# Kernel tuning notes

Hardware: AMD Instinct MI355X
Metric: run time of the kernel (lower is better)

## Reference

```python
import jax, jax.numpy as jnp
import numpy as np

VOCAB, EMB, HID = 120000, 64, 128
B, T = 256, 512


def _rnn_layer(inp, W_ih, b_ih, W_hh, b_hh):
    # inp: [B,T,D]. PyTorch RNN: h_t = tanh(W_ih x_t + b_ih + W_hh h_{t-1} + b_hh)
    pre = jnp.einsum('btd,hd->bth', inp, W_ih) + b_ih + b_hh  # input part hoisted out of scan
    h0 = jnp.zeros((inp.shape[0], W_hh.shape[0]), inp.dtype)

    def step(h, p_t):
        h = jnp.tanh(p_t + h @ W_hh.T)
        return h, h

    hT, outs = jax.lax.scan(step, h0, pre.transpose(1, 0, 2))  # scan over time
    return outs.transpose(1, 0, 2), hT  # [B,T,H], [B,H]


def _layernorm(x, g, b, eps=1e-5):
    mu = jnp.mean(x, axis=-1, keepdims=True)
    var = jnp.var(x, axis=-1, keepdims=True)
    return (x - mu) * jax.lax.rsqrt(var + eps) * g + b


def setup_inputs() -> dict:
    key = jax.random.key(0)
    ks = jax.random.split(key, 10)
    emb = jax.random.normal(ks[0], (VOCAB, EMB), jnp.float32) * 0.02
    emb = emb.at[0].set(0.0)  # padding_idx=0
    s_in, s_h = 1.0 / np.sqrt(HID), 1.0 / np.sqrt(HID)
    return {
        'x': jax.random.randint(ks[1], (B, T), 0, VOCAB),
        'emb': emb,
        'W_ih1': jax.random.normal(ks[2], (HID, EMB), jnp.float32) * s_in,
        'b_ih1': jnp.zeros((HID,), jnp.float32),
        'W_hh1': jax.random.normal(ks[3], (HID, HID), jnp.float32) * s_h,
        'b_hh1': jnp.zeros((HID,), jnp.float32),
        'W_ih2': jax.random.normal(ks[4], (HID, HID), jnp.float32) * s_in,
        'b_ih2': jnp.zeros((HID,), jnp.float32),
        'W_hh2': jax.random.normal(ks[5], (HID, HID), jnp.float32) * s_h,
        'b_hh2': jnp.zeros((HID,), jnp.float32),
        'ln_g': jnp.ones((HID,), jnp.float32),
        'ln_b': jnp.zeros((HID,), jnp.float32),
        'proj_W': jax.random.normal(ks[6], (HID, HID), jnp.float32) * s_h,
        'proj_b': jnp.zeros((HID,), jnp.float32),
        'on_g': jnp.ones((HID,), jnp.float32),
        'on_b': jnp.zeros((HID,), jnp.float32),
    }


def reference(x, emb, W_ih1, b_ih1, W_hh1, b_hh1, W_ih2, b_ih2, W_hh2, b_hh2,
              ln_g, ln_b, proj_W, proj_b, on_g, on_b):
    e = emb[x]                                   # [B,T,64]
    out1, _ = _rnn_layer(e, W_ih1, b_ih1, W_hh1, b_hh1)   # dropout is identity in eval
    _, h2 = _rnn_layer(out1, W_ih2, b_ih2, W_hh2, b_hh2)  # h2: [B,128] (last hidden state)
    rep = _layernorm(h2, ln_g, ln_b)
    rep = jnp.tanh(rep @ proj_W.T + proj_b)
    rep = _layernorm(rep, on_g, on_b)
    return rep
```

## Files before the change

### kernel.cpp

```cpp
#include <hip/hip_runtime.h>

#define BT (256*512)
#define HID 128
#define EMB 64
#define CH 32

__device__ __forceinline__ float fast_tanh(float x) {
    float e = __expf(2.f * x);
    return 1.f - __fdividef(2.f, e + 1.f);
}

#define OPQ(v) asm volatile("" : "+v"(v.x), "+v"(v.y), "+v"(v.z), "+v"(v.w))

#define DPPADD(v, ctrl) ((v) + __int_as_float(__builtin_amdgcn_mov_dpp(__float_as_int(v), (ctrl), 0xF, 0xF, false)))

#define RACC(P, Q, wa, wb, wc, wd) \
    P = fmaf(hv0.x, wa.x, P); Q = fmaf(hv0.y, wa.y, Q); \
    P = fmaf(hv0.z, wa.z, P); Q = fmaf(hv0.w, wa.w, Q); \
    P = fmaf(hv1.x, wb.x, P); Q = fmaf(hv1.y, wb.y, Q); \
    P = fmaf(hv1.z, wb.z, P); Q = fmaf(hv1.w, wb.w, Q); \
    P = fmaf(hv2.x, wc.x, P); Q = fmaf(hv2.y, wc.y, Q); \
    P = fmaf(hv2.z, wc.z, P); Q = fmaf(hv2.w, wc.w, Q); \
    P = fmaf(hv3.x, wd.x, P); Q = fmaf(hv3.y, wd.y, Q); \
    P = fmaf(hv3.z, wd.z, P); Q = fmaf(hv3.w, wd.w, Q);

__global__ __launch_bounds__(256)
__attribute__((amdgpu_waves_per_eu(1, 2)))
void k_embed_pre1(
    const int* __restrict__ x, const float* __restrict__ emb,
    const float* __restrict__ Wih1, const float* __restrict__ bih1,
    const float* __restrict__ bhh1, float* __restrict__ pre1)
{
    __shared__ float sA[32][128];
    __shared__ float sW[32][132];
    __shared__ int stok[128];
    const int tid = threadIdx.x;
    const int base = blockIdx.x * 128;
    const int tx = tid & 15, ty = tid >> 4;
    const int ox = tx * 8, py = ty * 8;
    const int pl = tid & 127, half = tid >> 7;
    if (tid < 128) stok[tid] = x[base + tid];
    float acc[8][8];
#pragma unroll
    for (int p = 0; p < 8; ++p)
#pragma unroll
        for (int o = 0; o < 8; ++o) acc[p][o] = 0.f;
    __syncthreads();
    const float4* ws = (const float4*)(Wih1 + (size_t)pl * EMB + half * 16);
    const float4* as = (const float4*)(emb + (size_t)stok[pl] * EMB + half * 16);
    float4 qw[2][4], qe[2][4];
#pragma unroll
    for (int kc = 0; kc < 2; ++kc)
#pragma unroll
        for (int k = 0; k < 4; ++k) {
            qw[kc][k] = ws[kc * 8 + k];
            qe[kc][k] = as[kc * 8 + k];
        }
    for (int kc = 0; kc < 2; ++kc) {
        {
            const int jb = half * 16;
#pragma unroll
            for (int k = 0; k < 4; ++k) {
                float4 q = qw[kc][k], e = qe[kc][k];
                sW[jb + 4*k + 0][pl] = q.x; sW[jb + 4*k + 1][pl] = q.y;
                sW[jb + 4*k + 2][pl] = q.z; sW[jb + 4*k + 3][pl] = q.w;
                sA[jb + 4*k + 0][pl] = e.x; sA[jb + 4*k + 1][pl] = e.y;
                sA[jb + 4*k + 2][pl] = e.z; sA[jb + 4*k + 3][pl] = e.w;
            }
        }
        __syncthreads();
#pragma unroll 4
        for (int j = 0; j < 32; ++j) {
            float4 a0 = *(const float4*)&sA[j][py];
            float4 a1 = *(const float4*)&sA[j][py + 4];
            float4 b0 = *(const float4*)&sW[j][ox];
            float4 b1 = *(const float4*)&sW[j][ox + 4];
            float av[8] = {a0.x,a0.y,a0.z,a0.w,a1.x,a1.y,a1.z,a1.w};
            float bv[8] = {b0.x,b0.y,b0.z,b0.w,b1.x,b1.y,b1.z,b1.w};
#pragma unroll
            for (int p = 0; p < 8; ++p)
#pragma unroll
                for (int o = 0; o < 8; ++o)
                    acc[p][o] = fmaf(av[p], bv[o], acc[p][o]);
        }
        __syncthreads();
    }
    float bo[8];
#pragma unroll
    for (int o = 0; o < 8; ++o) bo[o] = bih1[ox + o] + bhh1[ox + o];
#pragma unroll
    for (int p = 0; p < 8; ++p) {
        float* cp = pre1 + (size_t)(base + py + p) * HID + ox;
        *(float4*)cp       = make_float4(acc[p][0]+bo[0], acc[p][1]+bo[1], acc[p][2]+bo[2], acc[p][3]+bo[3]);
        *(float4*)(cp + 4) = make_float4(acc[p][4]+bo[4], acc[p][5]+bo[5], acc[p][6]+bo[6], acc[p][7]+bo[7]);
    }
}

__device__ inline float bsum768(float v, volatile float* sc, int tid) {
#pragma unroll
    for (int off = 32; off > 0; off >>= 1) v += __shfl_down(v, off, 64);
    __syncthreads();
    if ((tid & 63) == 0) sc[tid >> 6] = v;
    __syncthreads();
    float s = 0.f;
#pragma unroll
    for (int k = 0; k < 12; ++k) s += sc[k];
    return s;
}

__global__ __launch_bounds__(768)
__attribute__((amdgpu_waves_per_eu(1, 3)))
void k_rnn_fused(
    const float* __restrict__ pre1, const float* __restrict__ Whh1,
    const float* __restrict__ Wih2, const float* __restrict__ bih2,
    const float* __restrict__ bhh2, const float* __restrict__ Whh2,
    const float* __restrict__ ln_g, const float* __restrict__ ln_b,
    const float* __restrict__ projW, const float* __restrict__ proj_b,
    const float* __restrict__ on_g, const float* __restrict__ on_b,
    float* __restrict__ out)
{
    __shared__ __align__(16) float h1[2][160];
    __shared__ __align__(16) float h2[2][160];
    __shared__ __align__(16) float spre[CH * HID];
    __shared__ float sfin[HID];
    __shared__ float sc[12];

    const int bb   = blockIdx.x;
    const int tid  = threadIdx.x;
    const int w    = tid >> 6;
    const int lane = tid & 63;
    const bool L1  = (w < 4);
    const int  e   = lane & 7;
    const int  m   = L1 ? 0 : ((lane >> 3) & 1);
    const int  rg  = L1 ? (lane >> 3) : (lane >> 4);
    const int  rowbase = L1 ? (32 * w + rg) : (16 * (w - 4) + rg);
    const int  rstep   = L1 ? 8 : 4;
    const float* wmat  = L1 ? Whh1 : (m ? Whh2 : Wih2);

    const float4* wr0 = (const float4*)(wmat + (size_t)(rowbase            ) * HID + e * 16);
    const float4* wr1 = (const float4*)(wmat + (size_t)(rowbase +     rstep) * HID + e * 16);
    const float4* wr2 = (const float4*)(wmat + (size_t)(rowbase + 2 * rstep) * HID + e * 16);
    const float4* wr3 = (const float4*)(wmat + (size_t)(rowbase + 3 * rstep) * HID + e * 16);
    float4 w0 = wr0[0], w1 = wr0[1], w2  = wr0[2], w3  = wr0[3],
           w4 = wr1[0], w5 = wr1[1], w6  = wr1[2], w7  = wr1[3],
           w8 = wr2[0], w9 = wr2[1], w10 = wr2[2], w11 = wr2[3],
           w12= wr3[0], w13= wr3[1], w14 = wr3[2], w15 = wr3[3];
    OPQ(w0);OPQ(w1);OPQ(w2);OPQ(w3);OPQ(w4);OPQ(w5);OPQ(w6);OPQ(w7);
    OPQ(w8);OPQ(w9);OPQ(w10);OPQ(w11);OPQ(w12);OPQ(w13);OPQ(w14);OPQ(w15);

    const bool wr_en = L1 ? (e < 4) : (m == 0 && e < 4);
    const int  wrow  = rowbase + (e & 3) * rstep;
    const int  wword = ((wrow >> 4) * 20) + (wrow & 15);
    const float b2w  = (!L1 && wr_en) ? (bih2[wrow] + bhh2[wrow]) : 0.f;

    if (tid < 160) { h1[0][tid] = 0.f; h2[0][tid] = 0.f; }

    const float* srcb = (L1 || m == 0) ? &h1[0][0] : &h2[0][0];
    const float4* rp0 = (const float4*)(srcb + e * 20);
    const float4* rp1 = (const float4*)(srcb + 160 + e * 20);
    float* dstb = L1 ? &h1[0][0] : &h2[0][0];
    float* wp_e = dstb + 160 + wword;
    float* wp_o = dstb + wword;

    const float4* gsrc = (const float4*)(pre1 + (size_t)bb * 512 * HID);
    float4* spv = (float4*)spre;
    float4 pf0, pf1;
    if (tid < 512) { pf0 = gsrc[tid]; pf1 = gsrc[tid + 512]; }
    __syncthreads();

    auto do_step = [&](int t, int s, const float4* rp, float* wpt) {
        float4 hv0 = rp[0], hv1 = rp[1], hv2 = rp[2], hv3 = rp[3];
        float p0=0,q0=0,p1=0,q1=0,p2=0,q2=0,p3=0,q3=0;
        RACC(p0,q0, w0,w1,w2,w3)
        RACC(p1,q1, w4,w5,w6,w7)
        RACC(p2,q2, w8,w9,w10,w11)
        RACC(p3,q3, w12,w13,w14,w15)
        float s0 = p0+q0, s1 = p1+q1, s2 = p2+q2, s3 = p3+q3;
        s0 = DPPADD(s0, 0xB1); s1 = DPPADD(s1, 0xB1); s2 = DPPADD(s2, 0xB1); s3 = DPPADD(s3, 0xB1);
        s0 = DPPADD(s0, 0x4E); s1 = DPPADD(s1, 0x4E); s2 = DPPADD(s2, 0x4E); s3 = DPPADD(s3, 0x4E);
        s0 = DPPADD(s0, 0x141); s1 = DPPADD(s1, 0x141); s2 = DPPADD(s2, 0x141); s3 = DPPADD(s3, 0x141);
        if (!L1) {
            s0 = DPPADD(s0, 0x140); s1 = DPPADD(s1, 0x140);
            s2 = DPPADD(s2, 0x140); s3 = DPPADD(s3, 0x140);
        }
        if (wr_en) {
            float ta = (e & 1) ? s1 : s0;
            float tb = (e & 1) ? s3 : s2;
            float v  = (e & 2) ? tb : ta;
            if (L1) *wpt = fast_tanh(spre[s * HID + wrow] + v);
            else    *wpt = (t > 0) ? fast_tanh(b2w + v) : 0.f;
        }
        __syncthreads();
    };

#pragma unroll 1
    for (int c = 0; c < 512 / CH; ++c) {
        if (tid < 512) { spv[tid] = pf0; spv[tid + 512] = pf1; }
        __syncthreads();
        if (c < 512 / CH - 1 && tid < 512) {
            pf0 = gsrc[(c + 1) * 1024 + tid];
            pf1 = gsrc[(c + 1) * 1024 + tid + 512];
        }
        const int t0 = c * CH;
#pragma unroll 1
        for (int s = 0; s < CH; s += 2) {
            do_step(t0 + s,     s,     rp0, wp_e);
            do_step(t0 + s + 1, s + 1, rp1, wp_o);
        }
    }

    {
        float* wpD = L1 ? wp_e : &sfin[wrow];
        do_step(512, 0, rp0, wpD);
    }

    const int i = tid & 127;
    float hn = (tid < 128) ? sfin[i] : 0.f;
    float s1v = bsum768(hn, sc, tid);
    float s2v = bsum768(hn * hn, sc, tid);
    float mu = s1v * (1.f / 128.f);
    float var = s2v * (1.f / 128.f) - mu * mu;
    __syncthreads();
    if (tid < 128) spre[i] = (hn - mu) * rsqrtf(var + 1e-5f) * ln_g[i] + ln_b[i];
    __syncthreads();
    float pv = 0.f;
    if (tid < 128) {
        float a0 = proj_b[i], a1 = 0, a2 = 0, a3 = 0;
        const float4* hp = (const float4*)spre;
        const float4* pr = (const float4*)(projW + (size_t)i * HID);
#pragma unroll
        for (int k = 0; k < HID / 4; ++k) {
            float4 u = pr[k];
            float4 hv = hp[k];
            a0 = fmaf(hv.x, u.x, a0); a1 = fmaf(hv.y, u.y, a1);
            a2 = fmaf(hv.z, u.z, a2); a3 = fmaf(hv.w, u.w, a3);
        }
        pv = tanhf((a0 + a1) + (a2 + a3));
    }
    float t1 = bsum768(pv, sc, tid);
    float t2 = bsum768(pv * pv, sc, tid);
    float mu2 = t1 * (1.f / 128.f);
    float var2 = t2 * (1.f / 128.f) - mu2 * mu2;
    if (tid < 128)
        out[(size_t)bb * HID + i] = (pv - mu2) * rsqrtf(var2 + 1e-5f) * on_g[i] + on_b[i];
}

extern "C" void kernel_launch(void* const* d_in, const int* in_sizes, int n_in,
                              void* d_out, int out_size, void* d_ws, size_t ws_size,
                              hipStream_t stream)
{
    const int*   x     = (const int*)  d_in[0];
    const float* emb   = (const float*)d_in[1];
    const float* Wih1  = (const float*)d_in[2];
    const float* bih1  = (const float*)d_in[3];
    const float* Whh1  = (const float*)d_in[4];
    const float* bhh1  = (const float*)d_in[5];
    const float* Wih2  = (const float*)d_in[6];
    const float* bih2  = (const float*)d_in[7];
    const float* Whh2  = (const float*)d_in[8];
    const float* bhh2  = (const float*)d_in[9];
    const float* ln_g  = (const float*)d_in[10];
    const float* ln_b  = (const float*)d_in[11];
    const float* projW = (const float*)d_in[12];
    const float* projb = (const float*)d_in[13];
    const float* on_g  = (const float*)d_in[14];
    const float* on_b  = (const float*)d_in[15];

    float* pre1 = (float*)d_ws;

    k_embed_pre1<<<BT / 128, 256, 0, stream>>>(x, emb, Wih1, bih1, bhh1, pre1);
    k_rnn_fused<<<256, 768, 0, stream>>>(pre1, Whh1, Wih2, bih2, bhh2, Whh2,
                                         ln_g, ln_b, projW, projb, on_g, on_b,
                                         (float*)d_out);
}
```

Baseline: 447.9 us.

## Batch RNN scan across sequences with split-fp16 MFMA and pipelined layers

The recurrent scan now processes 16 sequences per block (16 blocks) using 16x16x32 fp16 MFMA. fp32 precision is emulated with hi/lo fp16 splits (three MFMAs per tile). The two layers and the layer-2 input projection run in separate wave roles, skewed in time and double-buffered in LDS. The pre1 layout is changed to time-major for coalesced per-step loads, and the layernorm/projection head moves to a separate kernel. This trades the per-sequence scalar FMA and DPP reductions for matrix-core throughput, but only 16 blocks run on a large GPU and there is a barrier every step.

```diff
diff --git a/kernel.cpp b/kernel.cpp
--- a/kernel.cpp
+++ b/kernel.cpp
@@ -3,26 +3,26 @@
 #define BT (256*512)
 #define HID 128
 #define EMB 64
-#define CH 32
+#define NB  16
+#define SEQ 16
+
+typedef _Float16 f16x4 __attribute__((ext_vector_type(4)));
+typedef _Float16 f16x8 __attribute__((ext_vector_type(8)));
+typedef float    f32x4 __attribute__((ext_vector_type(4)));
+
+#define MFMA(a, b, c) __builtin_amdgcn_mfma_f32_16x16x32_f16(a, b, c, 0, 0, 0)
+#define SHUF8(x, y) __builtin_shufflevector(x, y, 0, 1, 2, 3, 4, 5, 6, 7)
+#define TRRD(dst, a, OFF) asm volatile("ds_read_b64_tr_b16 %0, %1 offset:" OFF : "=v"(dst) : "v"(a))
+#define LDSR128(dst, a)   asm volatile("ds_read_b128 %0, %1" : "=v"(dst) : "v"(a))
 
 __device__ __forceinline__ float fast_tanh(float x) {
     float e = __expf(2.f * x);
     return 1.f - __fdividef(2.f, e + 1.f);
 }
 
-#define OPQ(v) asm volatile("" : "+v"(v.x), "+v"(v.y), "+v"(v.z), "+v"(v.w))
-
-#define DPPADD(v, ctrl) ((v) + __int_as_float(__builtin_amdgcn_mov_dpp(__float_as_int(v), (ctrl), 0xF, 0xF, false)))
-
-#define RACC(P, Q, wa, wb, wc, wd) \
-    P = fmaf(hv0.x, wa.x, P); Q = fmaf(hv0.y, wa.y, Q); \
-    P = fmaf(hv0.z, wa.z, P); Q = fmaf(hv0.w, wa.w, Q); \
-    P = fmaf(hv1.x, wb.x, P); Q = fmaf(hv1.y, wb.y, Q); \
-    P = fmaf(hv1.z, wb.z, P); Q = fmaf(hv1.w, wb.w, Q); \
-    P = fmaf(hv2.x, wc.x, P); Q = fmaf(hv2.y, wc.y, Q); \
-    P = fmaf(hv2.z, wc.z, P); Q = fmaf(hv2.w, wc.w, Q); \
-    P = fmaf(hv3.x, wd.x, P); Q = fmaf(hv3.y, wd.y, Q); \
-    P = fmaf(hv3.z, wd.z, P); Q = fmaf(hv3.w, wd.w, Q);
+__device__ __forceinline__ unsigned ldsoff(const void* p) {
+    return (unsigned)(unsigned long long)p;
+}
 
 __global__ __launch_bounds__(256)
 __attribute__((amdgpu_waves_per_eu(1, 2)))
@@ -90,159 +90,264 @@
     for (int o = 0; o < 8; ++o) bo[o] = bih1[ox + o] + bhh1[ox + o];
 #pragma unroll
     for (int p = 0; p < 8; ++p) {
-        float* cp = pre1 + (size_t)(base + py + p) * HID + ox;
+        const int pos = base + py + p;
+        const int bI = pos >> 9, tI = pos & 511;
+        float* cp = pre1 + ((size_t)tI * 256 + bI) * HID + ox;
         *(float4*)cp       = make_float4(acc[p][0]+bo[0], acc[p][1]+bo[1], acc[p][2]+bo[2], acc[p][3]+bo[3]);
         *(float4*)(cp + 4) = make_float4(acc[p][4]+bo[4], acc[p][5]+bo[5], acc[p][6]+bo[6], acc[p][7]+bo[7]);
     }
 }
 
-__device__ inline float bsum768(float v, volatile float* sc, int tid) {
-#pragma unroll
-    for (int off = 32; off > 0; off >>= 1) v += __shfl_down(v, off, 64);
-    __syncthreads();
-    if ((tid & 63) == 0) sc[tid >> 6] = v;
-    __syncthreads();
-    float s = 0.f;
-#pragma unroll
-    for (int k = 0; k < 12; ++k) s += sc[k];
-    return s;
-}
-
-__global__ __launch_bounds__(768)
-__attribute__((amdgpu_waves_per_eu(1, 3)))
-void k_rnn_fused(
-    const float* __restrict__ pre1, const float* __restrict__ Whh1,
+__global__ __launch_bounds__(384)
+__attribute__((amdgpu_waves_per_eu(2)))
+void k_rnn_scan(
+    const float* __restrict__ pre1T, const float* __restrict__ Whh1,
     const float* __restrict__ Wih2, const float* __restrict__ bih2,
     const float* __restrict__ bhh2, const float* __restrict__ Whh2,
-    const float* __restrict__ ln_g, const float* __restrict__ ln_b,
-    const float* __restrict__ projW, const float* __restrict__ proj_b,
-    const float* __restrict__ on_g, const float* __restrict__ on_b,
-    float* __restrict__ out)
+    float* __restrict__ h2fin)
 {
-    __shared__ __align__(16) float h1[2][160];
-    __shared__ __align__(16) float h2[2][160];
-    __shared__ __align__(16) float spre[CH * HID];
-    __shared__ float sfin[HID];
-    __shared__ float sc[12];
-
-    const int bb   = blockIdx.x;
+    __shared__ __align__(16) _Float16 hT[2][4][HID * SEQ];
+    __shared__ __align__(16) float    Pp[2][HID * SEQ];
+
     const int tid  = threadIdx.x;
-    const int w    = tid >> 6;
-    const int lane = tid & 63;
-    const bool L1  = (w < 4);
-    const int  e   = lane & 7;
-    const int  m   = L1 ? 0 : ((lane >> 3) & 1);
-    const int  rg  = L1 ? (lane >> 3) : (lane >> 4);
-    const int  rowbase = L1 ? (32 * w + rg) : (16 * (w - 4) + rg);
-    const int  rstep   = L1 ? 8 : 4;
-    const float* wmat  = L1 ? Whh1 : (m ? Whh2 : Wih2);
-
-    const float4* wr0 = (const float4*)(wmat + (size_t)(rowbase            ) * HID + e * 16);
-    const float4* wr1 = (const float4*)(wmat + (size_t)(rowbase +     rstep) * HID + e * 16);
-    const float4* wr2 = (const float4*)(wmat + (size_t)(rowbase + 2 * rstep) * HID + e * 16);
-    const float4* wr3 = (const float4*)(wmat + (size_t)(rowbase + 3 * rstep) * HID + e * 16);
-    float4 w0 = wr0[0], w1 = wr0[1], w2  = wr0[2], w3  = wr0[3],
-           w4 = wr1[0], w5 = wr1[1], w6  = wr1[2], w7  = wr1[3],
-           w8 = wr2[0], w9 = wr2[1], w10 = wr2[2], w11 = wr2[3],
-           w12= wr3[0], w13= wr3[1], w14 = wr3[2], w15 = wr3[3];
-    OPQ(w0);OPQ(w1);OPQ(w2);OPQ(w3);OPQ(w4);OPQ(w5);OPQ(w6);OPQ(w7);
-    OPQ(w8);OPQ(w9);OPQ(w10);OPQ(w11);OPQ(w12);OPQ(w13);OPQ(w14);OPQ(w15);
-
-    const bool wr_en = L1 ? (e < 4) : (m == 0 && e < 4);
-    const int  wrow  = rowbase + (e & 3) * rstep;
-    const int  wword = ((wrow >> 4) * 20) + (wrow & 15);
-    const float b2w  = (!L1 && wr_en) ? (bih2[wrow] + bhh2[wrow]) : 0.f;
-
-    if (tid < 160) { h1[0][tid] = 0.f; h2[0][tid] = 0.f; }
-
-    const float* srcb = (L1 || m == 0) ? &h1[0][0] : &h2[0][0];
-    const float4* rp0 = (const float4*)(srcb + e * 20);
-    const float4* rp1 = (const float4*)(srcb + 160 + e * 20);
-    float* dstb = L1 ? &h1[0][0] : &h2[0][0];
-    float* wp_e = dstb + 160 + wword;
-    float* wp_o = dstb + wword;
-
-    const float4* gsrc = (const float4*)(pre1 + (size_t)bb * 512 * HID);
-    float4* spv = (float4*)spre;
-    float4 pf0, pf1;
-    if (tid < 512) { pf0 = gsrc[tid]; pf1 = gsrc[tid + 512]; }
-    __syncthreads();
-
-    auto do_step = [&](int t, int s, const float4* rp, float* wpt) {
-        float4 hv0 = rp[0], hv1 = rp[1], hv2 = rp[2], hv3 = rp[3];
-        float p0=0,q0=0,p1=0,q1=0,p2=0,q2=0,p3=0,q3=0;
-        RACC(p0,q0, w0,w1,w2,w3)
-        RACC(p1,q1, w4,w5,w6,w7)
-        RACC(p2,q2, w8,w9,w10,w11)
-        RACC(p3,q3, w12,w13,w14,w15)
-        float s0 = p0+q0, s1 = p1+q1, s2 = p2+q2, s3 = p3+q3;
-        s0 = DPPADD(s0, 0xB1); s1 = DPPADD(s1, 0xB1); s2 = DPPADD(s2, 0xB1); s3 = DPPADD(s3, 0xB1);
-        s0 = DPPADD(s0, 0x4E); s1 = DPPADD(s1, 0x4E); s2 = DPPADD(s2, 0x4E); s3 = DPPADD(s3, 0x4E);
-        s0 = DPPADD(s0, 0x141); s1 = DPPADD(s1, 0x141); s2 = DPPADD(s2, 0x141); s3 = DPPADD(s3, 0x141);
-        if (!L1) {
-            s0 = DPPADD(s0, 0x140); s1 = DPPADD(s1, 0x140);
-            s2 = DPPADD(s2, 0x140); s3 = DPPADD(s3, 0x140);
-        }
-        if (wr_en) {
-            float ta = (e & 1) ? s1 : s0;
-            float tb = (e & 1) ? s3 : s2;
-            float v  = (e & 2) ? tb : ta;
-            if (L1) *wpt = fast_tanh(spre[s * HID + wrow] + v);
-            else    *wpt = (t > 0) ? fast_tanh(b2w + v) : 0.f;
+    const int w    = tid >> 6, lane = tid & 63;
+    const int role = w >> 1, half = w & 1;
+    const int col  = lane & 15;
+    const int kg   = lane >> 4;
+    const int sb   = kg * 4;
+    const int b0   = blockIdx.x * SEQ;
+
+    {
+        _Float16* z = &hT[0][0][0];
+        for (int i = tid; i < 4 * HID * SEQ; i += 384) z[i] = (_Float16)0.f;
+        for (int i = tid; i < HID * SEQ; i += 384) Pp[0][i] = 0.f;
+    }
+
+    const float* WM = (role == 0) ? Whh1 : ((role == 1) ? Wih2 : Whh2);
+    f16x8 bh[4][4], bl[4][4];
+    int outj[4];
+#pragma unroll
+    for (int j = 0; j < 4; ++j) {
+        const int out = (half * 4 + j) * 16 + col;
+        outj[j] = out;
+        const float* rp = WM + (size_t)out * HID + kg * 4;
+#pragma unroll
+        for (int kt = 0; kt < 4; ++kt) {
+            float4 a = *(const float4*)(rp + kt * 32);
+            float4 b4 = *(const float4*)(rp + kt * 32 + 16);
+            float v[8] = {a.x, a.y, a.z, a.w, b4.x, b4.y, b4.z, b4.w};
+            f16x8 hi, lo;
+#pragma unroll
+            for (int q = 0; q < 8; ++q) {
+                _Float16 h = (_Float16)v[q];
+                hi[q] = h;
+                lo[q] = (_Float16)(v[q] - (float)h);
+            }
+            bh[j][kt] = hi; bl[j][kt] = lo;
+        }
+    }
+    float b2j[4] = {0.f, 0.f, 0.f, 0.f};
+    if (role == 2) {
+#pragma unroll
+        for (int j = 0; j < 4; ++j) b2j[j] = bih2[outj[j]] + bhh2[outj[j]];
+    }
+
+    const unsigned hTb = ldsoff(&hT[0][0][0]);
+    const unsigned Ppb = ldsoff(&Pp[0][0]);
+    const int arr = (role == 2) ? 2 : 0;
+    const unsigned aHi0 = hTb + arr * 4096 + lane * 8;
+    const unsigned aHi1 = aHi0 + 16384;
+    int pjo[4];
+#pragma unroll
+    for (int j = 0; j < 4; ++j) pjo[j] = (outj[j] * 16 + sb) * 4;
+
+    float pc[4][4];
+    if (role == 0) {
+#pragma unroll
+        for (int j = 0; j < 4; ++j)
+#pragma unroll
+            for (int r = 0; r < 4; ++r)
+                pc[j][r] = pre1T[(size_t)(b0 + sb + r) * HID + outj[j]];
+    }
+    __syncthreads();
+
+    auto stepf = [&](int t, int rp) {
+        const int wp = rp ^ 1;
+        if (role == 0) {
+            if (t < 512) {
+                const unsigned ah = rp ? aHi1 : aHi0;
+                const unsigned al = ah + 4096;
+                f16x4 u0,u1,u2,u3,u4,u5,u6,u7, m0,m1,m2,m3,m4,m5,m6,m7;
+                TRRD(u0, ah, "0");    TRRD(u1, ah, "512");
+                TRRD(u2, ah, "1024"); TRRD(u3, ah, "1536");
+                TRRD(u4, ah, "2048"); TRRD(u5, ah, "2560");
+                TRRD(u6, ah, "3072"); TRRD(u7, ah, "3584");
+                TRRD(m0, al, "0");    TRRD(m1, al, "512");
+                TRRD(m2, al, "1024"); TRRD(m3, al, "1536");
+                TRRD(m4, al, "2048"); TRRD(m5, al, "2560");
+                TRRD(m6, al, "3072"); TRRD(m7, al, "3584");
+                asm volatile("s_waitcnt lgkmcnt(0)" ::: "memory");
+                __builtin_amdgcn_sched_barrier(0);
+                f16x8 Ah[4] = {SHUF8(u0,u1), SHUF8(u2,u3), SHUF8(u4,u5), SHUF8(u6,u7)};
+                f16x8 Al[4] = {SHUF8(m0,m1), SHUF8(m2,m3), SHUF8(m4,m5), SHUF8(m6,m7)};
+#pragma unroll
+                for (int j = 0; j < 4; ++j) {
+                    f32x4 c = {pc[j][0], pc[j][1], pc[j][2], pc[j][3]};
+#pragma unroll
+                    for (int kt = 0; kt < 4; ++kt) c = MFMA(Ah[kt], bh[j][kt], c);
+#pragma unroll
+                    for (int kt = 0; kt < 4; ++kt) c = MFMA(Al[kt], bh[j][kt], c);
+#pragma unroll
+                    for (int kt = 0; kt < 4; ++kt) c = MFMA(Ah[kt], bl[j][kt], c);
+                    f16x4 hi4, lo4;
+#pragma unroll
+                    for (int r = 0; r < 4; ++r) {
+                        float v = fast_tanh(c[r]);
+                        _Float16 h = (_Float16)v;
+                        hi4[r] = h;
+                        lo4[r] = (_Float16)(v - (float)h);
+                    }
+                    *(f16x4*)&hT[wp][0][outj[j] * 16 + sb] = hi4;
+                    *(f16x4*)&hT[wp][1][outj[j] * 16 + sb] = lo4;
+                }
+                const int tn = (t + 1 < 512) ? t + 1 : 511;
+                const size_t tb = (size_t)tn * 256 + b0 + sb;
+#pragma unroll
+                for (int j = 0; j < 4; ++j)
+#pragma unroll
+                    for (int r = 0; r < 4; ++r)
+                        pc[j][r] = pre1T[(tb + r) * HID + outj[j]];
+            }
+        } else if (role == 1) {
+            if (t < 513) {
+                const unsigned ah = rp ? aHi1 : aHi0;
+                const unsigned al = ah + 4096;
+                f16x4 u0,u1,u2,u3,u4,u5,u6,u7, m0,m1,m2,m3,m4,m5,m6,m7;
+                TRRD(u0, ah, "0");    TRRD(u1, ah, "512");
+                TRRD(u2, ah, "1024"); TRRD(u3, ah, "1536");
+                TRRD(u4, ah, "2048"); TRRD(u5, ah, "2560");
+                TRRD(u6, ah, "3072"); TRRD(u7, ah, "3584");
+                TRRD(m0, al, "0");    TRRD(m1, al, "512");
+                TRRD(m2, al, "1024"); TRRD(m3, al, "1536");
+                TRRD(m4, al, "2048"); TRRD(m5, al, "2560");
+                TRRD(m6, al, "3072"); TRRD(m7, al, "3584");
+                asm volatile("s_waitcnt lgkmcnt(0)" ::: "memory");
+                __builtin_amdgcn_sched_barrier(0);
+                f16x8 Ah[4] = {SHUF8(u0,u1), SHUF8(u2,u3), SHUF8(u4,u5), SHUF8(u6,u7)};
+                f16x8 Al[4] = {SHUF8(m0,m1), SHUF8(m2,m3), SHUF8(m4,m5), SHUF8(m6,m7)};
+#pragma unroll
+                for (int j = 0; j < 4; ++j) {
+                    f32x4 c = {0.f, 0.f, 0.f, 0.f};
+#pragma unroll
+                    for (int kt = 0; kt < 4; ++kt) c = MFMA(Ah[kt], bh[j][kt], c);
+#pragma unroll
+                    for (int kt = 0; kt < 4; ++kt) c = MFMA(Al[kt], bh[j][kt], c);
+#pragma unroll
+                    for (int kt = 0; kt < 4; ++kt) c = MFMA(Ah[kt], bl[j][kt], c);
+                    *(f32x4*)&Pp[wp][outj[j] * 16 + sb] = c;
+                }
+            }
+        } else {
+            const unsigned ah = rp ? aHi1 : aHi0;
+            const unsigned al = ah + 4096;
+            const unsigned pb = Ppb + rp * 8192;
+            f32x4 P0, P1, P2, P3;
+            LDSR128(P0, pb + pjo[0]); LDSR128(P1, pb + pjo[1]);
+            LDSR128(P2, pb + pjo[2]); LDSR128(P3, pb + pjo[3]);
+            f16x4 u0,u1,u2,u3,u4,u5,u6,u7, m0,m1,m2,m3,m4,m5,m6,m7;
+            TRRD(u0, ah, "0");    TRRD(u1, ah, "512");
+            TRRD(u2, ah, "1024"); TRRD(u3, ah, "1536");
+            TRRD(u4, ah, "2048"); TRRD(u5, ah, "2560");
+            TRRD(u6, ah, "3072"); TRRD(u7, ah, "3584");
+            TRRD(m0, al, "0");    TRRD(m1, al, "512");
+            TRRD(m2, al, "1024"); TRRD(m3, al, "1536");
+            TRRD(m4, al, "2048"); TRRD(m5, al, "2560");
+            TRRD(m6, al, "3072"); TRRD(m7, al, "3584");
+            asm volatile("s_waitcnt lgkmcnt(0)" ::: "memory");
+            __builtin_amdgcn_sched_barrier(0);
+            f16x8 Ah[4] = {SHUF8(u0,u1), SHUF8(u2,u3), SHUF8(u4,u5), SHUF8(u6,u7)};
+            f16x8 Al[4] = {SHUF8(m0,m1), SHUF8(m2,m3), SHUF8(m4,m5), SHUF8(m6,m7)};
+            f32x4 Pj[4] = {P0, P1, P2, P3};
+#pragma unroll
+            for (int j = 0; j < 4; ++j) {
+                f32x4 c;
+#pragma unroll
+                for (int r = 0; r < 4; ++r) c[r] = Pj[j][r] + b2j[j];
+#pragma unroll
+                for (int kt = 0; kt < 4; ++kt) c = MFMA(Ah[kt], bh[j][kt], c);
+#pragma unroll
+                for (int kt = 0; kt < 4; ++kt) c = MFMA(Al[kt], bh[j][kt], c);
+#pragma unroll
+                for (int kt = 0; kt < 4; ++kt) c = MFMA(Ah[kt], bl[j][kt], c);
+                if (t < 513) {
+                    f16x4 hi4, lo4;
+#pragma unroll
+                    for (int r = 0; r < 4; ++r) {
+                        float v = (t >= 2) ? fast_tanh(c[r]) : 0.f;
+                        _Float16 h = (_Float16)v;
+                        hi4[r] = h;
+                        lo4[r] = (_Float16)(v - (float)h);
+                    }
+                    *(f16x4*)&hT[wp][2][outj[j] * 16 + sb] = hi4;
+                    *(f16x4*)&hT[wp][3][outj[j] * 16 + sb] = lo4;
+                } else {
+#pragma unroll
+                    for (int r = 0; r < 4; ++r)
+                        h2fin[(size_t)(b0 + sb + r) * HID + outj[j]] = fast_tanh(c[r]);
+                }
+            }
         }
         __syncthreads();
     };
 
 #pragma unroll 1
-    for (int c = 0; c < 512 / CH; ++c) {
-        if (tid < 512) { spv[tid] = pf0; spv[tid + 512] = pf1; }
-        __syncthreads();
-        if (c < 512 / CH - 1 && tid < 512) {
-            pf0 = gsrc[(c + 1) * 1024 + tid];
-            pf1 = gsrc[(c + 1) * 1024 + tid + 512];
-        }
-        const int t0 = c * CH;
-#pragma unroll 1
-        for (int s = 0; s < CH; s += 2) {
-            do_step(t0 + s,     s,     rp0, wp_e);
-            do_step(t0 + s + 1, s + 1, rp1, wp_o);
-        }
-    }
-
-    {
-        float* wpD = L1 ? wp_e : &sfin[wrow];
-        do_step(512, 0, rp0, wpD);
-    }
-
-    const int i = tid & 127;
-    float hn = (tid < 128) ? sfin[i] : 0.f;
-    float s1v = bsum768(hn, sc, tid);
-    float s2v = bsum768(hn * hn, sc, tid);
-    float mu = s1v * (1.f / 128.f);
-    float var = s2v * (1.f / 128.f) - mu * mu;
-    __syncthreads();
-    if (tid < 128) spre[i] = (hn - mu) * rsqrtf(var + 1e-5f) * ln_g[i] + ln_b[i];
-    __syncthreads();
-    float pv = 0.f;
-    if (tid < 128) {
-        float a0 = proj_b[i], a1 = 0, a2 = 0, a3 = 0;
-        const float4* hp = (const float4*)spre;
-        const float4* pr = (const float4*)(projW + (size_t)i * HID);
-#pragma unroll
-        for (int k = 0; k < HID / 4; ++k) {
-            float4 u = pr[k];
-            float4 hv = hp[k];
-            a0 = fmaf(hv.x, u.x, a0); a1 = fmaf(hv.y, u.y, a1);
-            a2 = fmaf(hv.z, u.z, a2); a3 = fmaf(hv.w, u.w, a3);
-        }
-        pv = tanhf((a0 + a1) + (a2 + a3));
-    }
-    float t1 = bsum768(pv, sc, tid);
-    float t2 = bsum768(pv * pv, sc, tid);
-    float mu2 = t1 * (1.f / 128.f);
-    float var2 = t2 * (1.f / 128.f) - mu2 * mu2;
-    if (tid < 128)
-        out[(size_t)bb * HID + i] = (pv - mu2) * rsqrtf(var2 + 1e-5f) * on_g[i] + on_b[i];
+    for (int tt = 0; tt < 514; tt += 2) {
+        stepf(tt, 0);
+        stepf(tt + 1, 1);
+    }
+}
+
+__global__ __launch_bounds__(128)
+void k_head(const float* __restrict__ h2fin,
+            const float* __restrict__ ln_g, const float* __restrict__ ln_b,
+            const float* __restrict__ projW, const float* __restrict__ proj_b,
+            const float* __restrict__ on_g, const float* __restrict__ on_b,
+            float* __restrict__ out)
+{
+    __shared__ float xn[HID];
+    __shared__ float red[4];
+    const int b = blockIdx.x, i = threadIdx.x, wv = i >> 6;
+    float v = h2fin[(size_t)b * HID + i];
+    float sa = v, sq = v * v;
+#pragma unroll
+    for (int o = 32; o > 0; o >>= 1) { sa += __shfl_xor(sa, o, 64); sq += __shfl_xor(sq, o, 64); }
+    if ((i & 63) == 0) { red[wv * 2] = sa; red[wv * 2 + 1] = sq; }
+    __syncthreads();
+    float S = red[0] + red[2], Q = red[1] + red[3];
+    float mu = S * (1.f / 128.f), var = Q * (1.f / 128.f) - mu * mu;
+    float rs = rsqrtf(var + 1e-5f);
+    xn[i] = (v - mu) * rs * ln_g[i] + ln_b[i];
+    __syncthreads();
+    float a0 = proj_b[i], a1 = 0.f, a2 = 0.f, a3 = 0.f;
+    const float4* pr = (const float4*)(projW + (size_t)i * HID);
+    const float4* hp = (const float4*)xn;
+#pragma unroll
+    for (int k = 0; k < 32; ++k) {
+        float4 u = pr[k], h4 = hp[k];
+        a0 = fmaf(h4.x, u.x, a0); a1 = fmaf(h4.y, u.y, a1);
+        a2 = fmaf(h4.z, u.z, a2); a3 = fmaf(h4.w, u.w, a3);
+    }
+    float pv = tanhf((a0 + a1) + (a2 + a3));
+    float ta = pv, tq = pv * pv;
+#pragma unroll
+    for (int o = 32; o > 0; o >>= 1) { ta += __shfl_xor(ta, o, 64); tq += __shfl_xor(tq, o, 64); }
+    __syncthreads();
+    if ((i & 63) == 0) { red[wv * 2] = ta; red[wv * 2 + 1] = tq; }
+    __syncthreads();
+    float S2 = red[0] + red[2], Q2 = red[1] + red[3];
+    float mu2 = S2 * (1.f / 128.f), var2 = Q2 * (1.f / 128.f) - mu2 * mu2;
+    float rs2 = rsqrtf(var2 + 1e-5f);
+    out[(size_t)b * HID + i] = (pv - mu2) * rs2 * on_g[i] + on_b[i];
 }
 
 extern "C" void kernel_launch(void* const* d_in, const int* in_sizes, int n_in,
@@ -266,10 +371,11 @@
     const float* on_g  = (const float*)d_in[14];
     const float* on_b  = (const float*)d_in[15];
 
-    float* pre1 = (float*)d_ws;
+    float* pre1  = (float*)d_ws;
+    float* h2fin = pre1 + (size_t)511 * 256 * HID;
 
     k_embed_pre1<<<BT / 128, 256, 0, stream>>>(x, emb, Wih1, bih1, bhh1, pre1);
-    k_rnn_fused<<<256, 768, 0, stream>>>(pre1, Whh1, Wih2, bih2, bhh2, Whh2,
-                                         ln_g, ln_b, projW, projb, on_g, on_b,
-                                         (float*)d_out);
-}
+    k_rnn_scan<<<NB, 384, 0, stream>>>(pre1, Whh1, Wih2, bih2, bhh2, Whh2, h2fin);
+    k_head<<<256, 128, 0, stream>>>(h2fin, ln_g, ln_b, projW, projb, on_g, on_b,
+                                    (float*)d_out);
+}
```

New measurement: 1.259 ms. +181.2%, slower.

## Compute RNN recurrence with split-fp16 MFMA and a three-role pipeline

Applied to the files above, without the earlier changes.

Replaces the per-lane FP32 FMA dot products and DPP reductions in the fused RNN kernel with 16x16x32 fp16 MFMA instructions. Weights and hidden states are split into hi/lo fp16 halves, using three MFMAs per tile to approximate FP32 accuracy. Layer-2 input and recurrent projections are now handled by separate wave groups, with the W_ih2 result passed through a double-buffered Pp array. This adds one extra pipeline step at the end. The aim is to shorten the serial per-step matvec latency, at the cost of redundant MFMA work (only one output column is used) and some precision risk from the hi/lo split.

```diff
diff --git a/kernel.cpp b/kernel.cpp
--- a/kernel.cpp
+++ b/kernel.cpp
@@ -5,24 +5,14 @@
 #define EMB 64
 #define CH 32
 
+typedef _Float16 f16x8 __attribute__((ext_vector_type(8)));
+typedef float    f32x4 __attribute__((ext_vector_type(4)));
+#define MFMA(a, b, c) __builtin_amdgcn_mfma_f32_16x16x32_f16(a, b, c, 0, 0, 0)
+
 __device__ __forceinline__ float fast_tanh(float x) {
     float e = __expf(2.f * x);
     return 1.f - __fdividef(2.f, e + 1.f);
 }
-
-#define OPQ(v) asm volatile("" : "+v"(v.x), "+v"(v.y), "+v"(v.z), "+v"(v.w))
-
-#define DPPADD(v, ctrl) ((v) + __int_as_float(__builtin_amdgcn_mov_dpp(__float_as_int(v), (ctrl), 0xF, 0xF, false)))
-
-#define RACC(P, Q, wa, wb, wc, wd) \
-    P = fmaf(hv0.x, wa.x, P); Q = fmaf(hv0.y, wa.y, Q); \
-    P = fmaf(hv0.z, wa.z, P); Q = fmaf(hv0.w, wa.w, Q); \
-    P = fmaf(hv1.x, wb.x, P); Q = fmaf(hv1.y, wb.y, Q); \
-    P = fmaf(hv1.z, wb.z, P); Q = fmaf(hv1.w, wb.w, Q); \
-    P = fmaf(hv2.x, wc.x, P); Q = fmaf(hv2.y, wc.y, Q); \
-    P = fmaf(hv2.z, wc.z, P); Q = fmaf(hv2.w, wc.w, Q); \
-    P = fmaf(hv3.x, wd.x, P); Q = fmaf(hv3.y, wd.y, Q); \
-    P = fmaf(hv3.z, wd.z, P); Q = fmaf(hv3.w, wd.w, Q);
 
 __global__ __launch_bounds__(256)
 __attribute__((amdgpu_waves_per_eu(1, 2)))
@@ -109,7 +99,7 @@
 }
 
 __global__ __launch_bounds__(768)
-__attribute__((amdgpu_waves_per_eu(1, 3)))
+__attribute__((amdgpu_waves_per_eu(3)))
 void k_rnn_fused(
     const float* __restrict__ pre1, const float* __restrict__ Whh1,
     const float* __restrict__ Wih2, const float* __restrict__ bih2,
@@ -119,48 +109,60 @@
     const float* __restrict__ on_g, const float* __restrict__ on_b,
     float* __restrict__ out)
 {
-    __shared__ __align__(16) float h1[2][160];
-    __shared__ __align__(16) float h2[2][160];
-    __shared__ __align__(16) float spre[CH * HID];
+    __shared__ __align__(16) _Float16 h1h[2][HID], h1l[2][HID];
+    __shared__ __align__(16) _Float16 h2h[2][HID], h2l[2][HID];
+    __shared__ __align__(16) float    Pp[2][HID];
+    __shared__ __align__(16) float    spre[CH * HID];
     __shared__ float sfin[HID];
     __shared__ float sc[12];
 
     const int bb   = blockIdx.x;
     const int tid  = threadIdx.x;
-    const int w    = tid >> 6;
-    const int lane = tid & 63;
-    const bool L1  = (w < 4);
-    const int  e   = lane & 7;
-    const int  m   = L1 ? 0 : ((lane >> 3) & 1);
-    const int  rg  = L1 ? (lane >> 3) : (lane >> 4);
-    const int  rowbase = L1 ? (32 * w + rg) : (16 * (w - 4) + rg);
-    const int  rstep   = L1 ? 8 : 4;
-    const float* wmat  = L1 ? Whh1 : (m ? Whh2 : Wih2);
-
-    const float4* wr0 = (const float4*)(wmat + (size_t)(rowbase            ) * HID + e * 16);
-    const float4* wr1 = (const float4*)(wmat + (size_t)(rowbase +     rstep) * HID + e * 16);
-    const float4* wr2 = (const float4*)(wmat + (size_t)(rowbase + 2 * rstep) * HID + e * 16);
-    const float4* wr3 = (const float4*)(wmat + (size_t)(rowbase + 3 * rstep) * HID + e * 16);
-    float4 w0 = wr0[0], w1 = wr0[1], w2  = wr0[2], w3  = wr0[3],
-           w4 = wr1[0], w5 = wr1[1], w6  = wr1[2], w7  = wr1[3],
-           w8 = wr2[0], w9 = wr2[1], w10 = wr2[2], w11 = wr2[3],
-           w12= wr3[0], w13= wr3[1], w14 = wr3[2], w15 = wr3[3];
-    OPQ(w0);OPQ(w1);OPQ(w2);OPQ(w3);OPQ(w4);OPQ(w5);OPQ(w6);OPQ(w7);
-    OPQ(w8);OPQ(w9);OPQ(w10);OPQ(w11);OPQ(w12);OPQ(w13);OPQ(w14);OPQ(w15);
-
-    const bool wr_en = L1 ? (e < 4) : (m == 0 && e < 4);
-    const int  wrow  = rowbase + (e & 3) * rstep;
-    const int  wword = ((wrow >> 4) * 20) + (wrow & 15);
-    const float b2w  = (!L1 && wr_en) ? (bih2[wrow] + bhh2[wrow]) : 0.f;
-
-    if (tid < 160) { h1[0][tid] = 0.f; h2[0][tid] = 0.f; }
-
-    const float* srcb = (L1 || m == 0) ? &h1[0][0] : &h2[0][0];
-    const float4* rp0 = (const float4*)(srcb + e * 20);
-    const float4* rp1 = (const float4*)(srcb + 160 + e * 20);
-    float* dstb = L1 ? &h1[0][0] : &h2[0][0];
-    float* wp_e = dstb + 160 + wword;
-    float* wp_o = dstb + wword;
+    const int w    = tid >> 6, lane = tid & 63;
+    const int role = w >> 2;
+    const int tw   = w & 3;
+    const int col  = lane & 15;
+    const int kg   = lane >> 4;
+    const int out0 = (2 * tw) * 16 + col;
+    const int out1 = (2 * tw + 1) * 16 + col;
+
+    const float* WM = (role == 0) ? Whh1 : ((role == 1) ? Wih2 : Whh2);
+    f16x8 bh[2][4], bl[2][4];
+#pragma unroll
+    for (int j = 0; j < 2; ++j) {
+        const int oj = j ? out1 : out0;
+        const float* rw = WM + (size_t)oj * HID + kg * 8;
+#pragma unroll
+        for (int kt = 0; kt < 4; ++kt) {
+            float4 u0 = *(const float4*)(rw + kt * 32);
+            float4 u1 = *(const float4*)(rw + kt * 32 + 4);
+            float vv[8] = {u0.x,u0.y,u0.z,u0.w,u1.x,u1.y,u1.z,u1.w};
+            f16x8 hi, lo;
+#pragma unroll
+            for (int q = 0; q < 8; ++q) {
+                _Float16 hq = (_Float16)vv[q];
+                hi[q] = hq;
+                lo[q] = (_Float16)(vv[q] - (float)hq);
+            }
+            bh[j][kt] = hi; bl[j][kt] = lo;
+        }
+    }
+    float b20 = 0.f, b21 = 0.f;
+    if (role == 2) {
+        b20 = bih2[out0] + bhh2[out0];
+        b21 = bih2[out1] + bhh2[out1];
+    }
+
+    if (tid < 128) {
+        h1h[0][tid] = (_Float16)0.f; h1l[0][tid] = (_Float16)0.f;
+        h2h[0][tid] = (_Float16)0.f; h2l[0][tid] = (_Float16)0.f;
+        Pp[0][tid] = 0.f;
+    }
+
+    const f16x8* A0h = (role == 2) ? (const f16x8*)h2h[0] : (const f16x8*)h1h[0];
+    const f16x8* A0l = (role == 2) ? (const f16x8*)h2l[0] : (const f16x8*)h1l[0];
+    const f16x8* A1h = (role == 2) ? (const f16x8*)h2h[1] : (const f16x8*)h1h[1];
+    const f16x8* A1l = (role == 2) ? (const f16x8*)h2l[1] : (const f16x8*)h1l[1];
 
     const float4* gsrc = (const float4*)(pre1 + (size_t)bb * 512 * HID);
     float4* spv = (float4*)spre;
@@ -168,27 +170,61 @@
     if (tid < 512) { pf0 = gsrc[tid]; pf1 = gsrc[tid + 512]; }
     __syncthreads();
 
-    auto do_step = [&](int t, int s, const float4* rp, float* wpt) {
-        float4 hv0 = rp[0], hv1 = rp[1], hv2 = rp[2], hv3 = rp[3];
-        float p0=0,q0=0,p1=0,q1=0,p2=0,q2=0,p3=0,q3=0;
-        RACC(p0,q0, w0,w1,w2,w3)
-        RACC(p1,q1, w4,w5,w6,w7)
-        RACC(p2,q2, w8,w9,w10,w11)
-        RACC(p3,q3, w12,w13,w14,w15)
-        float s0 = p0+q0, s1 = p1+q1, s2 = p2+q2, s3 = p3+q3;
-        s0 = DPPADD(s0, 0xB1); s1 = DPPADD(s1, 0xB1); s2 = DPPADD(s2, 0xB1); s3 = DPPADD(s3, 0xB1);
-        s0 = DPPADD(s0, 0x4E); s1 = DPPADD(s1, 0x4E); s2 = DPPADD(s2, 0x4E); s3 = DPPADD(s3, 0x4E);
-        s0 = DPPADD(s0, 0x141); s1 = DPPADD(s1, 0x141); s2 = DPPADD(s2, 0x141); s3 = DPPADD(s3, 0x141);
-        if (!L1) {
-            s0 = DPPADD(s0, 0x140); s1 = DPPADD(s1, 0x140);
-            s2 = DPPADD(s2, 0x140); s3 = DPPADD(s3, 0x140);
-        }
-        if (wr_en) {
-            float ta = (e & 1) ? s1 : s0;
-            float tb = (e & 1) ? s3 : s2;
-            float v  = (e & 2) ? tb : ta;
-            if (L1) *wpt = fast_tanh(spre[s * HID + wrow] + v);
-            else    *wpt = (t > 0) ? fast_tanh(b2w + v) : 0.f;
+    auto stepf = [&](int t, int rp, int s) {
+        const int wp = rp ^ 1;
+        const bool active = (role == 0) ? (t < 512) : ((role == 1) ? (t < 513) : true);
+        if (active) {
+            const f16x8* Ah = rp ? A1h : A0h;
+            const f16x8* Al = rp ? A1l : A0l;
+            f16x8 ah0 = Ah[kg], ah1 = Ah[4 + kg], ah2 = Ah[8 + kg], ah3 = Ah[12 + kg];
+            f16x8 al0 = Al[kg], al1 = Al[4 + kg], al2 = Al[8 + kg], al3 = Al[12 + kg];
+            float i0, i1;
+            if (role == 0)      { i0 = spre[s * HID + out0]; i1 = spre[s * HID + out1]; }
+            else if (role == 1) { i0 = 0.f; i1 = 0.f; }
+            else                { i0 = Pp[rp][out0] + b20; i1 = Pp[rp][out1] + b21; }
+            f32x4 cA0 = {i0,i0,i0,i0}, cB0 = {0,0,0,0}, cC0 = {0,0,0,0};
+            f32x4 cA1 = {i1,i1,i1,i1}, cB1 = {0,0,0,0}, cC1 = {0,0,0,0};
+            cA0 = MFMA(ah0, bh[0][0], cA0); cA1 = MFMA(ah0, bh[1][0], cA1);
+            cB0 = MFMA(al0, bh[0][0], cB0); cB1 = MFMA(al0, bh[1][0], cB1);
+            cC0 = MFMA(ah0, bl[0][0], cC0); cC1 = MFMA(ah0, bl[1][0], cC1);
+            cA0 = MFMA(ah1, bh[0][1], cA0); cA1 = MFMA(ah1, bh[1][1], cA1);
+            cB0 = MFMA(al1, bh[0][1], cB0); cB1 = MFMA(al1, bh[1][1], cB1);
+            cC0 = MFMA(ah1, bl[0][1], cC0); cC1 = MFMA(ah1, bl[1][1], cC1);
+            cA0 = MFMA(ah2, bh[0][2], cA0); cA1 = MFMA(ah2, bh[1][2], cA1);
+            cB0 = MFMA(al2, bh[0][2], cB0); cB1 = MFMA(al2, bh[1][2], cB1);
+            cC0 = MFMA(ah2, bl[0][2], cC0); cC1 = MFMA(ah2, bl[1][2], cC1);
+            cA0 = MFMA(ah3, bh[0][3], cA0); cA1 = MFMA(ah3, bh[1][3], cA1);
+            cB0 = MFMA(al3, bh[0][3], cB0); cB1 = MFMA(al3, bh[1][3], cB1);
+            cC0 = MFMA(ah3, bl[0][3], cC0); cC1 = MFMA(ah3, bl[1][3], cC1);
+            float v0 = (cA0[0] + cB0[0]) + cC0[0];
+            float v1 = (cA1[0] + cB1[0]) + cC1[0];
+            if (role == 0) {
+                float q0 = fast_tanh(v0), q1 = fast_tanh(v1);
+                _Float16 H0 = (_Float16)q0, H1 = (_Float16)q1;
+                _Float16 L0 = (_Float16)(q0 - (float)H0);
+                _Float16 L1 = (_Float16)(q1 - (float)H1);
+                if (kg == 0) {
+                    h1h[wp][out0] = H0; h1l[wp][out0] = L0;
+                    h1h[wp][out1] = H1; h1l[wp][out1] = L1;
+                }
+            } else if (role == 1) {
+                if (kg == 0) { Pp[wp][out0] = v0; Pp[wp][out1] = v1; }
+            } else {
+                if (t < 513) {
+                    float q0 = (t >= 2) ? fast_tanh(v0) : 0.f;
+                    float q1 = (t >= 2) ? fast_tanh(v1) : 0.f;
+                    _Float16 H0 = (_Float16)q0, H1 = (_Float16)q1;
+                    _Float16 L0 = (_Float16)(q0 - (float)H0);
+                    _Float16 L1 = (_Float16)(q1 - (float)H1);
+                    if (kg == 0) {
+                        h2h[wp][out0] = H0; h2l[wp][out0] = L0;
+                        h2h[wp][out1] = H1; h2l[wp][out1] = L1;
+                    }
+                } else if (kg == 0) {
+                    sfin[out0] = fast_tanh(v0);
+                    sfin[out1] = fast_tanh(v1);
+                }
+            }
         }
         __syncthreads();
     };
@@ -204,15 +240,12 @@
         const int t0 = c * CH;
 #pragma unroll 1
         for (int s = 0; s < CH; s += 2) {
-            do_step(t0 + s,     s,     rp0, wp_e);
-            do_step(t0 + s + 1, s + 1, rp1, wp_o);
-        }
-    }
-
-    {
-        float* wpD = L1 ? wp_e : &sfin[wrow];
-        do_step(512, 0, rp0, wpD);
-    }
+            stepf(t0 + s,     0, s);
+            stepf(t0 + s + 1, 1, s + 1);
+        }
+    }
+    stepf(512, 0, 0);
+    stepf(513, 1, 0);
 
     const int i = tid & 127;
     float hn = (tid < 128) ? sfin[i] : 0.f;
```

New measurement: 622.7 us. 1.39x slower.
